# Kernel tuning notes

Hardware: AMD Instinct MI355X
Metric: run time of the kernel (lower is better)

The kernel has to match this reference:

```python
import jax, jax.numpy as jnp
import numpy as np

K = 3      # kernel size (hardcoded 3x3 in the torch module via repeat(...,9,...))
PAD = 1
STRIDE = 1


def _unfold(x):
    # torch.nn.functional.unfold equivalent: (B,C,H,W) -> (B,C,K,K,oh,ow)
    B, C, H, W = x.shape
    p = jax.lax.conv_general_dilated_patches(
        x, (K, K), (STRIDE, STRIDE), ((PAD, PAD), (PAD, PAD)))
    oh, ow = p.shape[2], p.shape[3]
    return p.reshape(B, C, K, K, oh, ow)


def setup_inputs() -> dict:
    key = jax.random.key(0)
    k1, k2, k3, k4 = jax.random.split(key, 4)
    B, Cin, Cout, H, W = 4, 64, 64, 128, 128
    inputs = jax.random.normal(k1, (B, Cin, H, W), jnp.float32)
    depth = jax.random.uniform(k2, (B, 1, H, W), jnp.float32)  # positive depths
    weight = jax.random.uniform(k3, (K, Cout, Cin, K, K), jnp.float32, minval=-0.05, maxval=0.05)
    bias = jax.random.uniform(k4, (Cout,), jnp.float32, minval=-0.05, maxval=0.05)
    return {"inputs": inputs, "depth": depth, "weight": weight, "bias": bias, "f": 1}


def reference(inputs, depth, weight, bias, f):
    # --- DepthKernelFn: per-depth-plane binary masks ---
    depth_wins = _unfold(depth)          # (B,1,K,K,oh,ow)
    s_wins = depth_wins / f              # grid spacing s_i = d / f
    cy, cx = K // 2, K // 2
    d0 = depth_wins[:, :, cy, cx]        # center depth      (B,1,oh,ow)
    s0 = s_wins[:, :, cy, cx]            # center spacing    (B,1,oh,ow)
    offs = jnp.arange(K, dtype=inputs.dtype) - (K - 1) / 2.0  # l - (K-1)/2
    # z_l at center: d0 + (l-1)*s0  -> (K,B,1,oh,ow)
    z0 = d0[None] + offs[:, None, None, None, None] * s0[None]
    half = s0[None] / 2
    a = (z0 - half)[:, :, :, None, None]  # (K,B,1,1,1,oh,ow)
    b = (z0 + half)[:, :, :, None, None]
    dw = depth_wins[None]                 # (1,B,1,K,K,oh,ow)
    # mask_l = 1 where a <= depth < b else 0  (same as the where-cascade in torch)
    mask = ((dw >= a) & (dw < b)).astype(inputs.dtype)  # (K,B,1,K,K,oh,ow)

    # --- RepeatKernelConvFn: masked windowed conv via einsum ---
    inp_wins = _unfold(inputs)            # (B,C,K,K,oh,ow)
    x = inp_wins[None] * mask             # (K,B,C,K,K,oh,ow), depth C=1 broadcasts
    out = jnp.einsum('hijklmn,hojkl->iomn', x, weight)
    out = out + bias.reshape(1, -1, 1, 1)
    return out
```

## Files before the change

kernel.cpp:

```cpp
#include <hip/hip_runtime.h>
#include <math.h>

#define B_N  4
#define CIN  64
#define COUT 64
#define H_N  128
#define W_N  128

typedef _Float16 half8 __attribute__((ext_vector_type(8)));
typedef float    f32x4 __attribute__((ext_vector_type(4)));

#define KTOT   1728
#define NSTEP  54
#define WA_BYTES ((size_t)NSTEP * 4 * 64 * 8 * 2)

__global__ void wprep(const float* __restrict__ w, _Float16* __restrict__ wa) {
    int idx = blockIdx.x * 256 + threadIdx.x;
    if (idx >= NSTEP * 4 * 64) return;
    int lane = idx & 63;
    int mt   = (idx >> 6) & 3;
    int s    = idx >> 8;
    int m    = mt * 16 + (lane & 15);
    int kl0  = (lane >> 4) * 8;
    _Float16 v[8];
#pragma unroll
    for (int j = 0; j < 8; ++j) {
        int k = s * 32 + kl0 + j;
        int g = k >> 6;
        int c = k & 63;
        int t = g / 3;
        int h = g % 3;
        v[j] = (_Float16)w[(((size_t)(h * COUT) + m) * CIN + c) * 9 + t];
    }
    *(int4*)&wa[(size_t)idx * 8] = *(int4*)v;
}

#define XS_STRIDE 72
#define XS_ROW    (130 * XS_STRIDE)

__global__ __launch_bounds__(256)
void conv_mfma(const float* __restrict__ inp, const float* __restrict__ depth,
               const _Float16* __restrict__ wa, const float* __restrict__ bias,
               const int* __restrict__ fptr, float* __restrict__ out) {
    __shared__ _Float16 Xs[3 * XS_ROW];

    int bid  = blockIdx.x;
    int y    = bid & (H_N - 1);
    int b    = bid >> 7;
    int tid  = threadIdx.x;
    int lane = tid & 63;
    int wid  = tid >> 6;
    int p0   = wid * 32;
    int ln15 = lane & 15;
    int quad = lane >> 4;

    {
        int x     = tid & 127;
        int chalf = tid >> 7;
        for (int dyi = 0; dyi < 3; ++dyi) {
            int yy = y + dyi - 1;
            _Float16 buf[32];
            if (yy >= 0 && yy < H_N) {
                const float* src = inp + (((size_t)b * CIN + chalf * 32) * H_N + yy) * W_N + x;
#pragma unroll
                for (int cc = 0; cc < 32; ++cc)
                    buf[cc] = (_Float16)src[(size_t)cc * H_N * W_N];
            } else {
#pragma unroll
                for (int cc = 0; cc < 32; ++cc) buf[cc] = (_Float16)0.f;
            }
            _Float16* dst = &Xs[dyi * XS_ROW + (x + 1) * XS_STRIDE + chalf * 32];
#pragma unroll
            for (int k = 0; k < 4; ++k)
                *(int4*)&dst[k * 8] = *(int4*)&buf[k * 8];
        }
        if (tid < 48) {
            int dyi = tid / 16;
            int rem = tid % 16;
            int xi  = (rem >= 8) ? 129 : 0;
            int k8  = rem & 7;
            int4 z  = {0, 0, 0, 0};
            *(int4*)&Xs[dyi * XS_ROW + xi * XS_STRIDE + k8 * 8] = z;
        }
    }

    double fd = (double)(*fptr);
    unsigned hpk[2];
#pragma unroll
    for (int nt = 0; nt < 2; ++nt) {
        int x = p0 + nt * 16 + ln15;
        float d0f = depth[((size_t)b * H_N + y) * W_N + x];
        double dd = (double)d0f;
        double s0 = dd / fd;
        unsigned pk = 0;
        for (int t = 0; t < 9; ++t) {
            int dy = t / 3 - 1, dx = t % 3 - 1;
            int yy = y + dy, xx = x + dx;
            float dwf = (yy >= 0 && yy < H_N && xx >= 0 && xx < W_N)
                        ? depth[((size_t)b * H_N + yy) * W_N + xx] : 0.f;
            int h = -1;
            if (s0 > 0.0) {
                double u  = ((double)dwf - dd) / s0 + 1.5;
                double uf = floor(u);
                if (uf >= 0.0 && uf <= 2.0) h = (int)uf;
            }
            pk |= (unsigned)(h + 1) << (2 * t);
        }
        hpk[nt] = pk;
    }

    __syncthreads();

    f32x4 acc[4][2];
#pragma unroll
    for (int mt = 0; mt < 4; ++mt)
#pragma unroll
        for (int nt = 0; nt < 2; ++nt) acc[mt][nt] = (f32x4){0.f, 0.f, 0.f, 0.f};

    const half8* wa8 = (const half8*)wa;

    for (int t = 0; t < 9; ++t) {
        int dyi = t / 3;
        int dx  = t % 3 - 1;
        int boff0 = dyi * XS_ROW + (p0 + 0  + ln15 + dx + 1) * XS_STRIDE + quad * 8;
        int boff1 = dyi * XS_ROW + (p0 + 16 + ln15 + dx + 1) * XS_STRIDE + quad * 8;
        int hb0 = (hpk[0] >> (2 * t)) & 3;
        int hb1 = (hpk[1] >> (2 * t)) & 3;

        half8 A[6][4];
        {
            const half8* base = wa8 + ((size_t)t * 6 * 4) * 64 + lane;
#pragma unroll
            for (int j = 0; j < 6; ++j)
#pragma unroll
                for (int mt = 0; mt < 4; ++mt)
                    A[j][mt] = base[(j * 4 + mt) * 64];
        }

#pragma unroll
        for (int h = 0; h < 3; ++h) {
            bool m0 = (hb0 == h + 1);
            bool m1 = (hb1 == h + 1);
#pragma unroll
            for (int kk = 0; kk < 2; ++kk) {
                int j = h * 2 + kk;
                half8 b0 = *(const half8*)&Xs[boff0 + kk * 32];
                half8 b1 = *(const half8*)&Xs[boff1 + kk * 32];
                half8 z  = {(_Float16)0.f, (_Float16)0.f, (_Float16)0.f, (_Float16)0.f,
                            (_Float16)0.f, (_Float16)0.f, (_Float16)0.f, (_Float16)0.f};
                b0 = m0 ? b0 : z;
                b1 = m1 ? b1 : z;
#pragma unroll
                for (int mt = 0; mt < 4; ++mt) {
                    acc[mt][0] = __builtin_amdgcn_mfma_f32_16x16x32_f16(A[j][mt], b0, acc[mt][0], 0, 0, 0);
                    acc[mt][1] = __builtin_amdgcn_mfma_f32_16x16x32_f16(A[j][mt], b1, acc[mt][1], 0, 0, 0);
                }
            }
        }
        __syncthreads();
    }

#pragma unroll
    for (int mt = 0; mt < 4; ++mt) {
#pragma unroll
        for (int nt = 0; nt < 2; ++nt) {
            int x = p0 + nt * 16 + ln15;
#pragma unroll
            for (int r = 0; r < 4; ++r) {
                int o = mt * 16 + quad * 4 + r;
                out[(((size_t)b * COUT + o) * H_N + y) * W_N + x] = acc[mt][nt][r] + bias[o];
            }
        }
    }
}

__global__ __launch_bounds__(256)
void conv25d(const float* __restrict__ inp, const float* __restrict__ depth,
             const float* __restrict__ wsrc, const float* __restrict__ bias,
             const int* __restrict__ fptr, float* __restrict__ out) {
    int bid = blockIdx.x;
    int xt  = bid & 3;
    int y   = (bid >> 2) & (H_N - 1);
    int b   = bid >> 9;
    int o   = threadIdx.x & 63;
    int q   = threadIdx.x >> 6;
    int x0  = xt * 32 + q * 8;
    double fd = (double)(*fptr);
    float acc[8];
    float bv = bias[o];
#pragma unroll
    for (int i = 0; i < 8; ++i) acc[i] = bv;
    const float* dcen = depth + ((size_t)b * H_N + y) * W_N;
    float d0[8];
#pragma unroll
    for (int i = 0; i < 8; ++i) d0[i] = dcen[x0 + i];
    for (int t = 0; t < 9; ++t) {
        int dy = t / 3 - 1, dx = t % 3 - 1;
        int yy = y + dy;
        if (yy < 0 || yy >= H_N) continue;
        const float* drow = depth + ((size_t)b * H_N + yy) * W_N;
        int hsel[8];
#pragma unroll
        for (int i = 0; i < 8; ++i) {
            int xx = x0 + i + dx;
            int h = -1;
            if (xx >= 0 && xx < W_N) {
                double dd = (double)d0[i];
                double s0 = dd / fd;
                if (s0 > 0.0) {
                    double u = ((double)drow[xx] - dd) / s0 + 1.5;
                    double uf = floor(u);
                    if (uf >= 0.0 && uf <= 2.0) h = (int)uf;
                }
            }
            hsel[i] = h;
        }
        const float* irow = inp + ((size_t)b * CIN * H_N + yy) * W_N;
        for (int c = 0; c < CIN; ++c) {
            const float* wb = wsrc + ((size_t)o * CIN + c) * 9 + t;
            float w0 = wb[0], w1 = wb[(size_t)COUT * CIN * 9], w2 = wb[2 * (size_t)COUT * CIN * 9];
            const float* ir = irow + (size_t)c * H_N * W_N;
#pragma unroll
            for (int i = 0; i < 8; ++i) {
                int h = hsel[i];
                if (h >= 0) {
                    float wv = (h == 0) ? w0 : ((h == 1) ? w1 : w2);
                    acc[i] = fmaf(ir[x0 + i + dx], wv, acc[i]);
                }
            }
        }
    }
    float* orow = out + (((size_t)b * COUT + o) * H_N + y) * W_N;
#pragma unroll
    for (int i = 0; i < 8; ++i) orow[x0 + i] = acc[i];
}

extern "C" void kernel_launch(void* const* d_in, const int* in_sizes, int n_in,
                              void* d_out, int out_size, void* d_ws, size_t ws_size,
                              hipStream_t stream) {
    const float* inp   = (const float*)d_in[0];
    const float* depth = (const float*)d_in[1];
    const float* w     = (const float*)d_in[2];
    const float* bias  = (const float*)d_in[3];
    const int*   f     = (const int*)d_in[4];
    float* out = (float*)d_out;

    if (ws_size >= WA_BYTES) {
        _Float16* wa = (_Float16*)d_ws;
        wprep<<<NSTEP, 256, 0, stream>>>(w, wa);
        conv_mfma<<<B_N * H_N, 256, 0, stream>>>(inp, depth, wa, bias, f, out);
    } else {
        conv25d<<<B_N * H_N * (W_N / 32), 256, 0, stream>>>(inp, depth, w, bias, f, out);
    }
}
```

Baseline: 105.5 us.

## Split conv tiles into half-row blocks with 2x2 wave M/N decomposition

Each block now handles half of an output row (64 pixels) instead of a full row, doubling the grid. Within a block the four waves split output channels and pixels 2x2, so each wave keeps fewer accumulators and weight fragments. The shared tile shrinks to 66 columns, launch bounds request 4 blocks per CU, and the redundant per-tap __syncthreads is removed. The trade-off is more halo reloads of input and depth, and redundant weight loads across waves that share a channel half.

```diff
diff --git a/kernel.cpp b/kernel.cpp
--- a/kernel.cpp
+++ b/kernel.cpp
@@ -36,51 +36,51 @@
 }
 
 #define XS_STRIDE 72
-#define XS_ROW    (130 * XS_STRIDE)
-
-__global__ __launch_bounds__(256)
+#define XS_ROW    (66 * XS_STRIDE)
+
+__global__ __launch_bounds__(256, 4)
 void conv_mfma(const float* __restrict__ inp, const float* __restrict__ depth,
                const _Float16* __restrict__ wa, const float* __restrict__ bias,
                const int* __restrict__ fptr, float* __restrict__ out) {
     __shared__ _Float16 Xs[3 * XS_ROW];
 
     int bid  = blockIdx.x;
-    int y    = bid & (H_N - 1);
-    int b    = bid >> 7;
+    int xh   = bid & 1;
+    int y    = (bid >> 1) & (H_N - 1);
+    int b    = bid >> 8;
+    int x0   = xh * 64;
     int tid  = threadIdx.x;
     int lane = tid & 63;
     int wid  = tid >> 6;
-    int p0   = wid * 32;
+    int mh   = wid & 1;
+    int nh   = wid >> 1;
     int ln15 = lane & 15;
     int quad = lane >> 4;
 
     {
-        int x     = tid & 127;
-        int chalf = tid >> 7;
-        for (int dyi = 0; dyi < 3; ++dyi) {
-            int yy = y + dyi - 1;
-            _Float16 buf[32];
-            if (yy >= 0 && yy < H_N) {
-                const float* src = inp + (((size_t)b * CIN + chalf * 32) * H_N + yy) * W_N + x;
-#pragma unroll
-                for (int cc = 0; cc < 32; ++cc)
-                    buf[cc] = (_Float16)src[(size_t)cc * H_N * W_N];
-            } else {
-#pragma unroll
-                for (int cc = 0; cc < 32; ++cc) buf[cc] = (_Float16)0.f;
-            }
-            _Float16* dst = &Xs[dyi * XS_ROW + (x + 1) * XS_STRIDE + chalf * 32];
-#pragma unroll
-            for (int k = 0; k < 4; ++k)
-                *(int4*)&dst[k * 8] = *(int4*)&buf[k * 8];
-        }
-        if (tid < 48) {
-            int dyi = tid / 16;
-            int rem = tid % 16;
-            int xi  = (rem >= 8) ? 129 : 0;
-            int k8  = rem & 7;
-            int4 z  = {0, 0, 0, 0};
-            *(int4*)&Xs[dyi * XS_ROW + xi * XS_STRIDE + k8 * 8] = z;
+        int xl0 = tid & 63;
+        int cq  = tid >> 6;
+#pragma unroll
+        for (int e = 0; e < 2; ++e) {
+            int xl = (e == 0) ? xl0 : 64 + xl0;
+            if (e == 1 && xl0 >= 2) break;
+            int gx = x0 - 1 + xl;
+            for (int dyi = 0; dyi < 3; ++dyi) {
+                int yy = y + dyi - 1;
+                _Float16 buf[16];
+                if (yy >= 0 && yy < H_N && gx >= 0 && gx < W_N) {
+                    const float* src = inp + (((size_t)b * CIN + cq * 16) * H_N + yy) * W_N + gx;
+#pragma unroll
+                    for (int cc = 0; cc < 16; ++cc)
+                        buf[cc] = (_Float16)src[(size_t)cc * H_N * W_N];
+                } else {
+#pragma unroll
+                    for (int cc = 0; cc < 16; ++cc) buf[cc] = (_Float16)0.f;
+                }
+                _Float16* dst = &Xs[dyi * XS_ROW + xl * XS_STRIDE + cq * 16];
+                *(int4*)&dst[0] = *(int4*)&buf[0];
+                *(int4*)&dst[8] = *(int4*)&buf[8];
+            }
         }
     }
 
@@ -88,7 +88,7 @@
     unsigned hpk[2];
 #pragma unroll
     for (int nt = 0; nt < 2; ++nt) {
-        int x = p0 + nt * 16 + ln15;
+        int x = x0 + nh * 32 + nt * 16 + ln15;
         float d0f = depth[((size_t)b * H_N + y) * W_N + x];
         double dd = (double)d0f;
         double s0 = dd / fd;
@@ -111,9 +111,9 @@
 
     __syncthreads();
 
-    f32x4 acc[4][2];
-#pragma unroll
-    for (int mt = 0; mt < 4; ++mt)
+    f32x4 acc[2][2];
+#pragma unroll
+    for (int mt = 0; mt < 2; ++mt)
 #pragma unroll
         for (int nt = 0; nt < 2; ++nt) acc[mt][nt] = (f32x4){0.f, 0.f, 0.f, 0.f};
 
@@ -122,18 +122,18 @@
     for (int t = 0; t < 9; ++t) {
         int dyi = t / 3;
         int dx  = t % 3 - 1;
-        int boff0 = dyi * XS_ROW + (p0 + 0  + ln15 + dx + 1) * XS_STRIDE + quad * 8;
-        int boff1 = dyi * XS_ROW + (p0 + 16 + ln15 + dx + 1) * XS_STRIDE + quad * 8;
+        int boff0 = dyi * XS_ROW + (nh * 32 + 0  + ln15 + dx + 1) * XS_STRIDE + quad * 8;
+        int boff1 = dyi * XS_ROW + (nh * 32 + 16 + ln15 + dx + 1) * XS_STRIDE + quad * 8;
         int hb0 = (hpk[0] >> (2 * t)) & 3;
         int hb1 = (hpk[1] >> (2 * t)) & 3;
 
-        half8 A[6][4];
+        half8 A[6][2];
         {
-            const half8* base = wa8 + ((size_t)t * 6 * 4) * 64 + lane;
+            const half8* base = wa8 + ((size_t)t * 6 * 4 + mh * 2) * 64 + lane;
 #pragma unroll
             for (int j = 0; j < 6; ++j)
 #pragma unroll
-                for (int mt = 0; mt < 4; ++mt)
+                for (int mt = 0; mt < 2; ++mt)
                     A[j][mt] = base[(j * 4 + mt) * 64];
         }
 
@@ -151,23 +151,22 @@
                 b0 = m0 ? b0 : z;
                 b1 = m1 ? b1 : z;
 #pragma unroll
-                for (int mt = 0; mt < 4; ++mt) {
+                for (int mt = 0; mt < 2; ++mt) {
                     acc[mt][0] = __builtin_amdgcn_mfma_f32_16x16x32_f16(A[j][mt], b0, acc[mt][0], 0, 0, 0);
                     acc[mt][1] = __builtin_amdgcn_mfma_f32_16x16x32_f16(A[j][mt], b1, acc[mt][1], 0, 0, 0);
                 }
             }
         }
-        __syncthreads();
-    }
-
-#pragma unroll
-    for (int mt = 0; mt < 4; ++mt) {
+    }
+
+#pragma unroll
+    for (int mt = 0; mt < 2; ++mt) {
 #pragma unroll
         for (int nt = 0; nt < 2; ++nt) {
-            int x = p0 + nt * 16 + ln15;
+            int x = x0 + nh * 32 + nt * 16 + ln15;
 #pragma unroll
             for (int r = 0; r < 4; ++r) {
-                int o = mt * 16 + quad * 4 + r;
+                int o = mh * 32 + mt * 16 + quad * 4 + r;
                 out[(((size_t)b * COUT + o) * H_N + y) * W_N + x] = acc[mt][nt][r] + bias[o];
             }
         }
@@ -248,7 +247,7 @@
     if (ws_size >= WA_BYTES) {
         _Float16* wa = (_Float16*)d_ws;
         wprep<<<NSTEP, 256, 0, stream>>>(w, wa);
-        conv_mfma<<<B_N * H_N, 256, 0, stream>>>(inp, depth, wa, bias, f, out);
+        conv_mfma<<<B_N * H_N * 2, 256, 0, stream>>>(inp, depth, wa, bias, f, out);
     } else {
         conv25d<<<B_N * H_N * (W_N / 32), 256, 0, stream>>>(inp, depth, w, bias, f, out);
     }
```

Measured after the change: 108.2 us. 2.6% more time.
